# Optimization experiments

Measured on AMD Instinct MI355X. Metric: run time of the kernel, lower is better.

## Reference

```python
import jax, jax.numpy as jnp
import numpy as np
from jax import lax

KSIZE = 7
SIGMA = 5.0
ALPHA = 0.05


def _gaussian_kernel(ksize: int, sigma: float) -> jnp.ndarray:
    # 2D Gaussian, normalized to sum 1, replicated depthwise for 3 channels: (3,1,k,k)
    ax = jnp.arange(ksize, dtype=jnp.float32) - (ksize - 1) / 2.0
    g1 = jnp.exp(-(ax ** 2) / (2.0 * sigma ** 2))
    g2 = jnp.outer(g1, g1)
    g2 = g2 / jnp.sum(g2)
    return jnp.broadcast_to(g2[None, None], (3, 1, ksize, ksize)).astype(jnp.float32)


def _sobel_kernel() -> jnp.ndarray:
    # (2,1,3,3): channel 0 -> Ix, channel 1 -> Iy
    sx = jnp.array([[-1.0, 0.0, 1.0], [-2.0, 0.0, 2.0], [-1.0, 0.0, 1.0]], dtype=jnp.float32)
    sy = sx.T
    return jnp.stack([sx[None], sy[None]], axis=0)  # (2,1,3,3)


def setup_inputs() -> dict:
    key = jax.random.key(0)
    x = jax.random.normal(key, (1, 1, 4096, 4096), dtype=jnp.float32)
    return {"x": x, "sobel_k": _sobel_kernel(), "gauss_k": _gaussian_kernel(KSIZE, SIGMA)}


def _conv(x, k, pad, groups):
    return lax.conv_general_dilated(
        x, k, window_strides=(1, 1), padding=[(pad, pad), (pad, pad)],
        dimension_numbers=("NCHW", "OIHW", "NCHW"), feature_group_count=groups)


def reference(x, sobel_k, gauss_k):
    # ImageGradientsLayer: Sobel conv -> (1,2,H,W)
    g = _conv(x, sobel_k, 1, 1)
    Ix, Iy = g[:, 0:1], g[:, 1:2]
    # ChannelProductLayer -> (1,3,H,W)
    prod = jnp.concatenate([Ix * Ix, Iy * Iy, Ix * Iy], axis=1)
    # SecondMomentMatrixLayer: depthwise Gaussian blur, groups=3
    S = _conv(prod, gauss_k, KSIZE // 2, 3)
    Sxx, Syy, Sxy = S[0, 0], S[0, 1], S[0, 2]
    # CornerResponseLayer: R = det - alpha*trace^2
    tr = Sxx + Syy
    R = (Sxx * Syy - Sxy * Sxy - ALPHA * tr * tr)[None, None]  # (1,1,H,W)
    # NMSLayer: median threshold, 7x7 maxpool (stride 1, pad 3), keep maxima
    med = jnp.median(R)
    Rt = jnp.where(R >= med, R, jnp.float32(0.0))
    mp = lax.reduce_window(Rt, -jnp.inf, lax.max, (1, 1, 7, 7), (1, 1, 1, 1),
                           [(0, 0), (0, 0), (3, 3), (3, 3)])
    out = jnp.where(Rt != mp, jnp.float32(0.0), mp)
    return out
```

## Files before the change

kernel.cpp:

```cpp
#include <hip/hip_runtime.h>
#include <math.h>

#define N_IMG 4096
#define NBC   1024
#define H_OUT 32
#define HR    38
#define NPIX  (N_IMG * N_IMG)

struct W7 { float w[7]; };

__device__ __forceinline__ unsigned f2k(float f) {
    unsigned u = __float_as_uint(f);
    return (u & 0x80000000u) ? ~u : (u | 0x80000000u);
}
__device__ __forceinline__ float k2f(unsigned k) {
    unsigned u = (k & 0x80000000u) ? (k & 0x7fffffffu) : ~k;
    return __uint_as_float(u);
}

struct SelState { unsigned p1, p2, r1, r2; };

template<int BINS>
__device__ void locate_pair(const unsigned* __restrict__ h0,
                            const unsigned* __restrict__ h1,
                            int shift, SelState& s)
{
    __shared__ unsigned scan[256];
    __shared__ unsigned resb[2], resr[2];
    const int tid = threadIdx.x;
    const int per = BINS / 256;
    const bool same = (h0 == h1);

    for (int q = 0; q < 2; q++) {
        if (q == 1 && same) break;
        const unsigned* __restrict__ h = q ? h1 : h0;
        const int base = tid * per;
        unsigned sum = 0;
        #pragma unroll
        for (int i = 0; i < per; i++) sum += h[base + i];
        __syncthreads();
        scan[tid] = sum;
        __syncthreads();
        unsigned v = sum;
        #pragma unroll
        for (int off = 1; off < 256; off <<= 1) {
            unsigned t = (tid >= off) ? scan[tid - off] : 0u;
            __syncthreads();
            v += t;
            scan[tid] = v;
            __syncthreads();
        }
        const unsigned excl = v - sum;
        #pragma unroll
        for (int w = 0; w < 2; w++) {
            const unsigned rank = w ? s.r2 : s.r1;
            const bool mine = w ? (same || q == 1) : (q == 0);
            if (mine && rank >= excl && rank < v) {
                unsigned rr = rank - excl;
                for (int i = 0; i < per; i++) {
                    unsigned c = h[base + i];
                    if (rr < c) { resb[w] = (unsigned)(base + i); resr[w] = rr; break; }
                    rr -= c;
                }
            }
        }
        __syncthreads();
    }
    s.p1 |= resb[0] << shift; s.r1 = resr[0];
    s.p2 |= resb[1] << shift; s.r2 = resr[1];
}

__device__ __forceinline__ SelState derive0(const unsigned* __restrict__ g0) {
    SelState s; s.p1 = 0u; s.p2 = 0u;
    s.r1 = (unsigned)(NPIX / 2 - 1); s.r2 = (unsigned)(NPIX / 2);
    locate_pair<4096>(g0, g0, 20, s);
    return s;
}
__device__ __forceinline__ void derive1(const unsigned* __restrict__ g1, SelState& s) {
    const unsigned* h1 = (s.p1 != s.p2) ? (g1 + 4096) : g1;
    locate_pair<4096>(g1, h1, 8, s);
}
__device__ __forceinline__ void derive2(const unsigned* __restrict__ g2, SelState& s) {
    const unsigned* h1 = (s.p1 != s.p2) ? (g2 + 256) : g2;
    locate_pair<256>(g2, h1, 0, s);
}

__global__ __launch_bounds__(256, 2) void harris_kernel(const float* __restrict__ x,
                                                        float* __restrict__ R,
                                                        unsigned* __restrict__ g0,
                                                        W7 wp)
{
    __shared__ unsigned histo[4096];
    const int tid = threadIdx.x;
    for (int i = tid; i < 4096; i += 256) histo[i] = 0;
    __syncthreads();

    const int row0 = blockIdx.y * H_OUT;
    const int jc   = blockIdx.x * NBC + tid * 4;
    const float* w = wp.w;
    const bool edge = (jc < 4) || (jc >= N_IMG - 8);

    float xm[12], xc[12], xp[12];
    float axx[7][4], ayy[7][4], axy[7][4];

    #pragma unroll
    for (int m = 0; m < 7; m++)
        #pragma unroll
        for (int o = 0; o < 4; o++) { axx[m][o] = 0.f; ayy[m][o] = 0.f; axy[m][o] = 0.f; }

    auto loadrow = [&](int ri, float* d) {
        if ((unsigned)ri < N_IMG) {
            const float* p = x + (size_t)ri * N_IMG;
            float4 v0 = make_float4(0.f,0.f,0.f,0.f), v2 = make_float4(0.f,0.f,0.f,0.f);
            if (jc >= 4) v0 = *(const float4*)(p + jc - 4);
            float4 v1 = *(const float4*)(p + jc);
            if (jc + 4 < N_IMG) v2 = *(const float4*)(p + jc + 4);
            d[0]=v0.x; d[1]=v0.y; d[2]=v0.z; d[3]=v0.w;
            d[4]=v1.x; d[5]=v1.y; d[6]=v1.z; d[7]=v1.w;
            d[8]=v2.x; d[9]=v2.y; d[10]=v2.z; d[11]=v2.w;
        } else {
            #pragma unroll
            for (int t = 0; t < 12; t++) d[t] = 0.f;
        }
    };

    loadrow(row0 - 4, xm);
    loadrow(row0 - 3, xc);

    int curb = -1; unsigned cnt = 0;

    auto step = [&](int r, int k, int dmin, bool emit) {
        const int ri = row0 + r - 3;
        loadrow(ri + 1, xp);

        if ((unsigned)ri < N_IMG) {
            float dc[12], rd[12];
            #pragma unroll
            for (int t = 0; t < 12; t++) {
                dc[t] = xm[t] + 2.f * xc[t] + xp[t];
                rd[t] = xp[t] - xm[t];
            }
            float ixv[10], iyv[10];
            #pragma unroll
            for (int t = 0; t < 10; t++) {
                ixv[t] = dc[t+2] - dc[t];
                iyv[t] = rd[t] + 2.f * rd[t+1] + rd[t+2];
            }
            if (edge) {
                #pragma unroll
                for (int t = 0; t < 10; t++)
                    if ((unsigned)(jc - 3 + t) >= N_IMG) { ixv[t] = 0.f; iyv[t] = 0.f; }
            }
            float sxx[4] = {0,0,0,0}, syy[4] = {0,0,0,0}, sxy[4] = {0,0,0,0};
            #pragma unroll
            for (int t = 0; t < 10; t++) {
                float ix = ixv[t], iy = iyv[t];
                float xx = ix*ix, yy = iy*iy, xy = ix*iy;
                #pragma unroll
                for (int o = 0; o < 4; o++) {
                    const int v = t - o;
                    if (v >= 0 && v < 7) {
                        sxx[o] = fmaf(w[v], xx, sxx[o]);
                        syy[o] = fmaf(w[v], yy, syy[o]);
                        sxy[o] = fmaf(w[v], xy, sxy[o]);
                    }
                }
            }
            #pragma unroll
            for (int d = 0; d < 7; d++) {
                if (d >= dmin) {
                    const int m = (k + d) % 7;
                    #pragma unroll
                    for (int o = 0; o < 4; o++) {
                        axx[m][o] = fmaf(w[6-d], sxx[o], axx[m][o]);
                        ayy[m][o] = fmaf(w[6-d], syy[o], ayy[m][o]);
                        axy[m][o] = fmaf(w[6-d], sxy[o], axy[m][o]);
                    }
                }
            }
        }

        if (emit) {
            float4 h;
            float* hp = &h.x;
            #pragma unroll
            for (int o = 0; o < 4; o++) {
                float ax = axx[k][o], ay = ayy[k][o], az = axy[k][o];
                axx[k][o] = 0.f; ayy[k][o] = 0.f; axy[k][o] = 0.f;
                float tr = ax + ay;
                hp[o] = ax*ay - az*az - 0.05f*tr*tr;
            }
            const int orow = row0 + r - 6;
            *(float4*)(R + (size_t)orow * N_IMG + jc) = h;
            #pragma unroll
            for (int o = 0; o < 4; o++) {
                int b = (int)(f2k(hp[o]) >> 20);
                if (b == curb) cnt++;
                else { if (curb >= 0) atomicAdd(&histo[curb], cnt); curb = b; cnt = 1; }
            }
        }
        #pragma unroll
        for (int t = 0; t < 12; t++) { xm[t] = xc[t]; xc[t] = xp[t]; }
    };

    #pragma unroll
    for (int rr = 0; rr < 7; ++rr)
        step(rr, rr, 6 - rr, rr == 6);
    for (int it = 1; it < 6; ++it) {
        #pragma unroll
        for (int k = 0; k < 7; ++k) {
            const int r = it * 7 + k;
            if (r < HR) step(r, k, 0, true);
        }
    }

    if (curb >= 0) atomicAdd(&histo[curb], cnt);
    __syncthreads();
    for (int i = tid; i < 4096; i += 256) {
        unsigned c = histo[i];
        if (c) atomicAdd(&g0[i], c);
    }
}

__global__ __launch_bounds__(256) void hist1_kernel(const float* __restrict__ R,
                                                    const unsigned* __restrict__ g0,
                                                    unsigned* __restrict__ g1)
{
    __shared__ unsigned h[2][4096];
    const int tid = threadIdx.x;
    for (int i = tid; i < 8192; i += 256) ((unsigned*)h)[i] = 0u;

    SelState s = derive0(g0);
    const unsigned p1 = s.p1, p2 = s.p2;
    const bool dual = (p1 != p2);
    const unsigned mask = 0xFFF00000u;
    const int shift = 8;

    const int n4 = NPIX / 4;
    int curb1 = -1; unsigned cnt1 = 0;
    int curb2 = -1; unsigned cnt2 = 0;
    const float4* R4 = (const float4*)R;
    for (int i = blockIdx.x * 256 + tid; i < n4; i += gridDim.x * 256) {
        float4 v = R4[i];
        float vv[4] = {v.x, v.y, v.z, v.w};
        #pragma unroll
        for (int t = 0; t < 4; t++) {
            unsigned k = f2k(vv[t]);
            if ((k & mask) == p1) {
                int b = (int)((k >> shift) & 4095u);
                if (b == curb1) cnt1++;
                else { if (cnt1) atomicAdd(&h[0][curb1], cnt1); curb1 = b; cnt1 = 1; }
            }
            if (dual && (k & mask) == p2) {
                int b = (int)((k >> shift) & 4095u);
                if (b == curb2) cnt2++;
                else { if (cnt2) atomicAdd(&h[1][curb2], cnt2); curb2 = b; cnt2 = 1; }
            }
        }
    }
    if (cnt1) atomicAdd(&h[0][curb1], cnt1);
    if (cnt2) atomicAdd(&h[1][curb2], cnt2);
    __syncthreads();
    for (int i = tid; i < 4096; i += 256) {
        unsigned c0 = h[0][i]; if (c0) atomicAdd(&g1[i], c0);
        if (dual) { unsigned c1 = h[1][i]; if (c1) atomicAdd(&g1[4096 + i], c1); }
    }
}

__global__ __launch_bounds__(256) void hist2_kernel(const float* __restrict__ R,
                                                    const unsigned* __restrict__ g0,
                                                    const unsigned* __restrict__ g1,
                                                    unsigned* __restrict__ g2)
{
    __shared__ unsigned h[2][256];
    const int tid = threadIdx.x;
    for (int i = tid; i < 512; i += 256) ((unsigned*)h)[i] = 0u;

    SelState s = derive0(g0);
    derive1(g1, s);
    const unsigned p1 = s.p1, p2 = s.p2;
    const bool dual = (p1 != p2);
    const unsigned mask = 0xFFFFFF00u;

    const int n4 = NPIX / 4;
    int curb1 = -1; unsigned cnt1 = 0;
    int curb2 = -1; unsigned cnt2 = 0;
    const float4* R4 = (const float4*)R;
    for (int i = blockIdx.x * 256 + tid; i < n4; i += gridDim.x * 256) {
        float4 v = R4[i];
        float vv[4] = {v.x, v.y, v.z, v.w};
        #pragma unroll
        for (int t = 0; t < 4; t++) {
            unsigned k = f2k(vv[t]);
            if ((k & mask) == p1) {
                int b = (int)(k & 255u);
                if (b == curb1) cnt1++;
                else { if (cnt1) atomicAdd(&h[0][curb1], cnt1); curb1 = b; cnt1 = 1; }
            }
            if (dual && (k & mask) == p2) {
                int b = (int)(k & 255u);
                if (b == curb2) cnt2++;
                else { if (cnt2) atomicAdd(&h[1][curb2], cnt2); curb2 = b; cnt2 = 1; }
            }
        }
    }
    if (cnt1) atomicAdd(&h[0][curb1], cnt1);
    if (cnt2) atomicAdd(&h[1][curb2], cnt2);
    __syncthreads();
    if (tid < 256) {
        unsigned c0 = h[0][tid]; if (c0) atomicAdd(&g2[tid], c0);
        if (dual) { unsigned c1 = h[1][tid]; if (c1) atomicAdd(&g2[256 + tid], c1); }
    }
}

__global__ __launch_bounds__(256) void init_kernel(unsigned* __restrict__ g)
{
    const int tid = threadIdx.x;
    for (int i = tid; i < 16384; i += 256) g[i] = 0u;
}

__global__ __launch_bounds__(256, 2) void nms_kernel(const float* __restrict__ R,
                                                     const unsigned* __restrict__ g0,
                                                     const unsigned* __restrict__ g1,
                                                     const unsigned* __restrict__ g2,
                                                     float* __restrict__ out)
{
    const int tid  = threadIdx.x;

    SelState s = derive0(g0);
    derive1(g1, s);
    derive2(g2, s);
    const float med = 0.5f * (k2f(s.p1) + k2f(s.p2));

    const int row0 = blockIdx.y * H_OUT;
    const int jc   = blockIdx.x * NBC + tid * 4;

    float vm[7][4];
    float ct[7][4];
    #pragma unroll
    for (int m = 0; m < 7; m++)
        #pragma unroll
        for (int o = 0; o < 4; o++) vm[m][o] = -INFINITY;

    auto loadrowT = [&](int ri, float* d) {
        if ((unsigned)ri < N_IMG) {
            const float* p = R + (size_t)ri * N_IMG;
            float4 v1 = *(const float4*)(p + jc);
            d[4] = (v1.x >= med) ? v1.x : 0.f;
            d[5] = (v1.y >= med) ? v1.y : 0.f;
            d[6] = (v1.z >= med) ? v1.z : 0.f;
            d[7] = (v1.w >= med) ? v1.w : 0.f;
            if (jc >= 4) {
                float4 v0 = *(const float4*)(p + jc - 4);
                d[0] = (v0.x >= med) ? v0.x : 0.f;
                d[1] = (v0.y >= med) ? v0.y : 0.f;
                d[2] = (v0.z >= med) ? v0.z : 0.f;
                d[3] = (v0.w >= med) ? v0.w : 0.f;
            } else { d[0]=d[1]=d[2]=d[3] = -INFINITY; }
            if (jc + 4 < N_IMG) {
                float4 v2 = *(const float4*)(p + jc + 4);
                d[8]  = (v2.x >= med) ? v2.x : 0.f;
                d[9]  = (v2.y >= med) ? v2.y : 0.f;
                d[10] = (v2.z >= med) ? v2.z : 0.f;
                d[11] = (v2.w >= med) ? v2.w : 0.f;
            } else { d[8]=d[9]=d[10]=d[11] = -INFINITY; }
        } else {
            #pragma unroll
            for (int t = 0; t < 12; t++) d[t] = -INFINITY;
        }
    };

    auto stepn = [&](int r, int k, int dmin, bool emit) {
        const int ri = row0 + r - 3;
        float a[12];
        loadrowT(ri, a);
        float hm[4];
        #pragma unroll
        for (int o = 0; o < 4; o++) {
            float m01 = fmaxf(a[o+1], a[o+2]);
            float m23 = fmaxf(a[o+3], a[o+4]);
            float m45 = fmaxf(a[o+5], a[o+6]);
            hm[o] = fmaxf(fmaxf(m01, m23), fmaxf(m45, a[o+7]));
            ct[k][o] = a[4+o];
        }
        #pragma unroll
        for (int d = 0; d < 7; d++) {
            if (d >= dmin) {
                const int m = (k + d) % 7;
                #pragma unroll
                for (int o = 0; o < 4; o++)
                    vm[m][o] = fmaxf(vm[m][o], hm[o]);
            }
        }
        if (emit) {
            float4 ov;
            float* op = &ov.x;
            #pragma unroll
            for (int o = 0; o < 4; o++) {
                float m = vm[k][o];
                vm[k][o] = -INFINITY;
                float c = ct[(k+4) % 7][o];
                op[o] = (c != m) ? 0.f : m;
            }
            const int orow = row0 + r - 6;
            *(float4*)(out + (size_t)orow * N_IMG + jc) = ov;
        }
    };

    #pragma unroll
    for (int rr = 0; rr < 7; ++rr)
        stepn(rr, rr, 6 - rr, rr == 6);
    for (int it = 1; it < 6; ++it) {
        #pragma unroll
        for (int k = 0; k < 7; ++k) {
            const int r = it * 7 + k;
            if (r < HR) stepn(r, k, 0, true);
        }
    }
}

extern "C" void kernel_launch(void* const* d_in, const int* in_sizes, int n_in,
                              void* d_out, int out_size, void* d_ws, size_t ws_size,
                              hipStream_t stream)
{
    const float* x = (const float*)d_in[0];
    float* R = (float*)d_ws;
    unsigned* g0 = (unsigned*)((char*)d_ws + (size_t)N_IMG * N_IMG * 4);
    unsigned* g1 = g0 + 4096;
    unsigned* g2 = g1 + 8192;
    float* out = (float*)d_out;

    W7 wp;
    {
        double g[7], sm = 0.0;
        for (int i = 0; i < 7; i++) { double ax = (double)i - 3.0; g[i] = exp(-(ax*ax)/50.0); sm += g[i]; }
        for (int i = 0; i < 7; i++) wp.w[i] = (float)(g[i] / sm);
    }

    dim3 sgrid(N_IMG / NBC, N_IMG / H_OUT);

    init_kernel<<<1, 256, 0, stream>>>(g0);
    harris_kernel<<<sgrid, 256, 0, stream>>>(x, R, g0, wp);
    hist1_kernel<<<2048, 256, 0, stream>>>(R, g0, g1);
    hist2_kernel<<<2048, 256, 0, stream>>>(R, g0, g1, g2);
    nms_kernel<<<sgrid, 256, 0, stream>>>(R, g0, g1, g2, out);
}
```

Baseline: 289.1 us.

## Replace two refinement histogram passes with one fine 20-bit histogram pass

The median radix select previously made two extra full passes over R (a 12-bit and then an 8-bit refinement). It now makes one pass that builds a 1M-bin global histogram of the low 20 key bits inside the median's coarse bucket, plus a 4096-bin coarse summary. When the two middle ranks fall in different top buckets, it records a max/min instead. The harris and NMS kernels also prefetch one row ahead so loads overlap compute. The cost is zeroing a 4 MB histogram and heavy global atomics if many pixels land in the median bucket; the old path remains as a fallback when the workspace is too small.

```diff
diff --git a/kernel.cpp b/kernel.cpp
--- a/kernel.cpp
+++ b/kernel.cpp
@@ -6,6 +6,7 @@
 #define H_OUT 32
 #define HR    38
 #define NPIX  (N_IMG * N_IMG)
+#define FINE_BINS (1u << 20)
 
 struct W7 { float w[7]; };
 
@@ -21,8 +22,7 @@
 struct SelState { unsigned p1, p2, r1, r2; };
 
 template<int BINS>
-__device__ void locate_pair(const unsigned* __restrict__ h0,
-                            const unsigned* __restrict__ h1,
+__device__ void locate_pair(const unsigned* h0, const unsigned* h1,
                             int shift, SelState& s)
 {
     __shared__ unsigned scan[256];
@@ -33,7 +33,7 @@
 
     for (int q = 0; q < 2; q++) {
         if (q == 1 && same) break;
-        const unsigned* __restrict__ h = q ? h1 : h0;
+        const unsigned* h = q ? h1 : h0;
         const int base = tid * per;
         unsigned sum = 0;
         #pragma unroll
@@ -70,19 +70,27 @@
     s.p2 |= resb[1] << shift; s.r2 = resr[1];
 }
 
-__device__ __forceinline__ SelState derive0(const unsigned* __restrict__ g0) {
+__device__ __forceinline__ SelState derive0(const unsigned* g0) {
     SelState s; s.p1 = 0u; s.p2 = 0u;
     s.r1 = (unsigned)(NPIX / 2 - 1); s.r2 = (unsigned)(NPIX / 2);
     locate_pair<4096>(g0, g0, 20, s);
     return s;
 }
-__device__ __forceinline__ void derive1(const unsigned* __restrict__ g1, SelState& s) {
+__device__ __forceinline__ void derive1_old(const unsigned* g1, SelState& s) {
     const unsigned* h1 = (s.p1 != s.p2) ? (g1 + 4096) : g1;
     locate_pair<4096>(g1, h1, 8, s);
 }
-__device__ __forceinline__ void derive2(const unsigned* __restrict__ g2, SelState& s) {
+__device__ __forceinline__ void derive2_old(const unsigned* g2, SelState& s) {
     const unsigned* h1 = (s.p1 != s.p2) ? (g2 + 256) : g2;
     locate_pair<256>(g2, h1, 0, s);
+}
+__device__ __forceinline__ void derive_coarse(const unsigned* coarse, SelState& s) {
+    locate_pair<4096>(coarse, coarse, 8, s);
+}
+__device__ __forceinline__ void derive_fine(const unsigned* fine, SelState& s) {
+    const unsigned* f1 = fine + (((s.p1 >> 8) & 0xFFFu) << 8);
+    const unsigned* f2 = fine + (((s.p2 >> 8) & 0xFFFu) << 8);
+    locate_pair<256>(f1, f2, 0, s);
 }
 
 __global__ __launch_bounds__(256, 2) void harris_kernel(const float* __restrict__ x,
@@ -100,7 +108,7 @@
     const float* w = wp.w;
     const bool edge = (jc < 4) || (jc >= N_IMG - 8);
 
-    float xm[12], xc[12], xp[12];
+    float xm[12], xc[12], xp[12], xn[12];
     float axx[7][4], ayy[7][4], axy[7][4];
 
     #pragma unroll
@@ -126,12 +134,13 @@
 
     loadrow(row0 - 4, xm);
     loadrow(row0 - 3, xc);
+    loadrow(row0 - 2, xp);
 
     int curb = -1; unsigned cnt = 0;
 
     auto step = [&](int r, int k, int dmin, bool emit) {
         const int ri = row0 + r - 3;
-        loadrow(ri + 1, xp);
+        loadrow(ri + 2, xn);
 
         if ((unsigned)ri < N_IMG) {
             float dc[12], rd[12];
@@ -200,7 +209,7 @@
             }
         }
         #pragma unroll
-        for (int t = 0; t < 12; t++) { xm[t] = xc[t]; xc[t] = xp[t]; }
+        for (int t = 0; t < 12; t++) { xm[t] = xc[t]; xc[t] = xp[t]; xp[t] = xn[t]; }
     };
 
     #pragma unroll
@@ -220,6 +229,49 @@
         unsigned c = histo[i];
         if (c) atomicAdd(&g0[i], c);
     }
+}
+
+__global__ __launch_bounds__(256) void hist_fine_kernel(const float* __restrict__ R,
+                                                        const unsigned* __restrict__ g0,
+                                                        unsigned* __restrict__ coarse,
+                                                        unsigned* __restrict__ fine,
+                                                        unsigned* __restrict__ mm)
+{
+    SelState s = derive0(g0);
+    const unsigned p1 = s.p1, p2 = s.p2;
+    const bool dual = (p1 != p2);
+    const unsigned mask = 0xFFF00000u;
+    const int tid = threadIdx.x;
+    const int n4 = NPIX / 4;
+    const float4* R4 = (const float4*)R;
+    for (int i = blockIdx.x * 256 + tid; i < n4; i += gridDim.x * 256) {
+        float4 v = R4[i];
+        float vv[4] = {v.x, v.y, v.z, v.w};
+        #pragma unroll
+        for (int t = 0; t < 4; t++) {
+            unsigned k = f2k(vv[t]);
+            unsigned pref = k & mask;
+            if (!dual) {
+                if (pref == p1) {
+                    unsigned lo = k & 0xFFFFFu;
+                    atomicAdd(&fine[lo], 1u);
+                    atomicAdd(&coarse[lo >> 8], 1u);
+                }
+            } else {
+                if (pref == p1) atomicMax(&mm[0], k);
+                if (pref == p2) atomicMin(&mm[1], k);
+            }
+        }
+    }
+}
+
+__global__ __launch_bounds__(256) void init_fine_kernel(unsigned* __restrict__ g0,
+                                                        unsigned* __restrict__ mm)
+{
+    const unsigned n = 4096u + 4096u + FINE_BINS;
+    for (unsigned i = blockIdx.x * 256u + threadIdx.x; i < n; i += gridDim.x * 256u)
+        g0[i] = 0u;
+    if (blockIdx.x == 0 && threadIdx.x == 0) { mm[0] = 0u; mm[1] = 0xFFFFFFFFu; }
 }
 
 __global__ __launch_bounds__(256) void hist1_kernel(const float* __restrict__ R,
@@ -277,7 +329,7 @@
     for (int i = tid; i < 512; i += 256) ((unsigned*)h)[i] = 0u;
 
     SelState s = derive0(g0);
-    derive1(g1, s);
+    derive1_old(g1, s);
     const unsigned p1 = s.p1, p2 = s.p2;
     const bool dual = (p1 != p2);
     const unsigned mask = 0xFFFFFF00u;
@@ -313,30 +365,47 @@
     }
 }
 
-__global__ __launch_bounds__(256) void init_kernel(unsigned* __restrict__ g)
+__global__ __launch_bounds__(256) void init_old_kernel(unsigned* __restrict__ g)
 {
     const int tid = threadIdx.x;
     for (int i = tid; i < 16384; i += 256) g[i] = 0u;
 }
 
+template<int MODE>
 __global__ __launch_bounds__(256, 2) void nms_kernel(const float* __restrict__ R,
                                                      const unsigned* __restrict__ g0,
                                                      const unsigned* __restrict__ g1,
                                                      const unsigned* __restrict__ g2,
+                                                     const unsigned* __restrict__ coarse,
+                                                     const unsigned* __restrict__ fine,
+                                                     const unsigned* __restrict__ mm,
                                                      float* __restrict__ out)
 {
     const int tid  = threadIdx.x;
 
     SelState s = derive0(g0);
-    derive1(g1, s);
-    derive2(g2, s);
-    const float med = 0.5f * (k2f(s.p1) + k2f(s.p2));
+    float med;
+    if (MODE == 1) {
+        const bool dual0 = (s.p1 != s.p2);
+        if (dual0) {
+            med = 0.5f * (k2f(mm[0]) + k2f(mm[1]));
+        } else {
+            derive_coarse(coarse, s);
+            derive_fine(fine, s);
+            med = 0.5f * (k2f(s.p1) + k2f(s.p2));
+        }
+    } else {
+        derive1_old(g1, s);
+        derive2_old(g2, s);
+        med = 0.5f * (k2f(s.p1) + k2f(s.p2));
+    }
 
     const int row0 = blockIdx.y * H_OUT;
     const int jc   = blockIdx.x * NBC + tid * 4;
 
     float vm[7][4];
     float ct[7][4];
+    float a[12], an[12];
     #pragma unroll
     for (int m = 0; m < 7; m++)
         #pragma unroll
@@ -370,10 +439,11 @@
         }
     };
 
+    loadrowT(row0 - 3, a);
+
     auto stepn = [&](int r, int k, int dmin, bool emit) {
         const int ri = row0 + r - 3;
-        float a[12];
-        loadrowT(ri, a);
+        loadrowT(ri + 1, an);
         float hm[4];
         #pragma unroll
         for (int o = 0; o < 4; o++) {
@@ -405,6 +475,8 @@
             const int orow = row0 + r - 6;
             *(float4*)(out + (size_t)orow * N_IMG + jc) = ov;
         }
+        #pragma unroll
+        for (int t = 0; t < 12; t++) a[t] = an[t];
     };
 
     #pragma unroll
@@ -425,9 +497,7 @@
 {
     const float* x = (const float*)d_in[0];
     float* R = (float*)d_ws;
-    unsigned* g0 = (unsigned*)((char*)d_ws + (size_t)N_IMG * N_IMG * 4);
-    unsigned* g1 = g0 + 4096;
-    unsigned* g2 = g1 + 8192;
+    unsigned* g0 = (unsigned*)((char*)d_ws + (size_t)NPIX * 4);
     float* out = (float*)d_out;
 
     W7 wp;
@@ -439,9 +509,26 @@
 
     dim3 sgrid(N_IMG / NBC, N_IMG / H_OUT);
 
-    init_kernel<<<1, 256, 0, stream>>>(g0);
-    harris_kernel<<<sgrid, 256, 0, stream>>>(x, R, g0, wp);
-    hist1_kernel<<<2048, 256, 0, stream>>>(R, g0, g1);
-    hist2_kernel<<<2048, 256, 0, stream>>>(R, g0, g1, g2);
-    nms_kernel<<<sgrid, 256, 0, stream>>>(R, g0, g1, g2, out);
-}
+    const size_t need_fine = (size_t)NPIX * 4 +
+                             (size_t)(4096 + 4096 + FINE_BINS + 64) * 4;
+
+    if (ws_size >= need_fine) {
+        unsigned* coarse = g0 + 4096;
+        unsigned* fine   = coarse + 4096;
+        unsigned* mm     = fine + FINE_BINS;
+        init_fine_kernel<<<1024, 256, 0, stream>>>(g0, mm);
+        harris_kernel<<<sgrid, 256, 0, stream>>>(x, R, g0, wp);
+        hist_fine_kernel<<<2048, 256, 0, stream>>>(R, g0, coarse, fine, mm);
+        nms_kernel<1><<<sgrid, 256, 0, stream>>>(R, g0, nullptr, nullptr,
+                                                 coarse, fine, mm, out);
+    } else {
+        unsigned* g1 = g0 + 4096;
+        unsigned* g2 = g1 + 8192;
+        init_old_kernel<<<1, 256, 0, stream>>>(g0);
+        harris_kernel<<<sgrid, 256, 0, stream>>>(x, R, g0, wp);
+        hist1_kernel<<<2048, 256, 0, stream>>>(R, g0, g1);
+        hist2_kernel<<<2048, 256, 0, stream>>>(R, g0, g1, g2);
+        nms_kernel<0><<<sgrid, 256, 0, stream>>>(R, g0, g1, g2,
+                                                 nullptr, nullptr, nullptr, out);
+    }
+}
```

Measured after the change: 339.5 us. 1.17x slower.
